# Optimization experiments

Hardware: AMD Instinct MI355X
Metric: run time of the kernel (lower is better)

## Reference

```python
import jax, jax.numpy as jnp
import numpy as np

B, T, HID, H = 2, 2048, 2048, 16
D = HID // H  # 128


def apply_rope(x):
    # Faithful port of the torch helper: treats x dims as (B, T, H, D)
    # regardless of the caller's actual layout (this reproduces the
    # original module's quirk of rotating q along the head axis).
    b, t, h, d = x.shape
    half = d // 2
    x1, x2 = x[..., :half], x[..., half:]
    theta = 1.0 / (10000.0 ** (jnp.arange(0, half, 2, dtype=jnp.float32) / half))
    pos = jnp.arange(t, dtype=jnp.float32)
    freq = pos[:, None] * theta[None, :]            # (t, half//2)
    sin = jnp.sin(freq)[None, :, None, :]
    cos = jnp.cos(freq)[None, :, None, :]
    x1e, x1o = x1[..., ::2], x1[..., 1::2]
    x2e, x2o = x2[..., ::2], x2[..., 1::2]
    x1r = jnp.concatenate([x1e * cos - x1o * sin, x1e * sin + x1o * cos], axis=-1)
    x2r = jnp.concatenate([x2e * cos - x2o * sin, x2e * sin + x2o * cos], axis=-1)
    return jnp.concatenate([x1r, x2r], axis=-1)


def setup_inputs() -> dict:
    key = jax.random.key(0)
    ks = jax.random.split(key, 5)
    s = 0.02
    return {
        "hidden_states": jax.random.normal(ks[0], (B, T, HID), dtype=jnp.float32),
        "Wq": jax.random.normal(ks[1], (HID, HID), dtype=jnp.float32) * s,
        "Wk": jax.random.normal(ks[2], (D, HID), dtype=jnp.float32) * s,
        "Wv": jax.random.normal(ks[3], (D, HID), dtype=jnp.float32) * s,
        "Wo": jax.random.normal(ks[4], (HID, HID), dtype=jnp.float32) * s,
    }


def reference(hidden_states, Wq, Wk, Wv, Wo):
    b, t, _ = hidden_states.shape
    scaling = D ** -0.5
    # projections (nn.Linear: x @ W.T)
    q = (hidden_states @ Wq.T).reshape(b, t, H, D).transpose(0, 2, 1, 3)  # (B,H,T,D)
    k = hidden_states @ Wk.T                                             # (B,T,D)
    v = hidden_states @ Wv.T                                             # (B,T,D)
    # RoPE applied exactly as in the torch module (note layout quirk)
    q = apply_rope(q)                 # rotated along head axis, as original
    k = apply_rope(k[:, None])        # (B,1,T,D): pos=0 -> permutation only
    v = v[:, None]                    # (B,1,T,D)
    scores = jnp.einsum("bhqd,bokd->bhqk", q, k) * scaling  # (B,H,T,T)
    causal = jnp.tril(jnp.ones((t, t), dtype=bool))
    scores = jnp.where(causal[None, None], scores, -jnp.inf)
    probs = jax.nn.softmax(scores, axis=-1)
    attn = jnp.einsum("bhqk,bokd->bhqd", probs, v)           # (B,H,T,D)
    attn = attn.transpose(0, 2, 1, 3).reshape(b, t, HID)
    return attn @ Wo.T
```

## Files before the change

kernel.cpp:

```cpp
#include <hip/hip_runtime.h>
#include <math.h>


typedef unsigned short u16;
typedef __attribute__((ext_vector_type(8))) short s16x8;
typedef __attribute__((ext_vector_type(4))) float f32x4;

#define B_   2
#define T_   2048
#define HID_ 2048
#define H_   16
#define D_   128

__device__ __forceinline__ u16 f2bf(float f) {
  unsigned u = __float_as_uint(f);
  unsigned r = ((u >> 16) & 1u) + 0x7fffu;
  return (u16)((u + r) >> 16);
}
__device__ __forceinline__ float bf2f(u16 b) {
  return __uint_as_float(((unsigned)b) << 16);
}

__global__ void cast_f32_to_bf16(const float* __restrict__ in,
                                 u16* __restrict__ out, int n4) {
  int i = blockIdx.x * blockDim.x + threadIdx.x;
  if (i >= n4) return;
  float4 v = reinterpret_cast<const float4*>(in)[i];
  ushort4 o;
  o.x = f2bf(v.x); o.y = f2bf(v.y); o.z = f2bf(v.z); o.w = f2bf(v.w);
  reinterpret_cast<ushort4*>(out)[i] = o;
}

__device__ __forceinline__ void gload_lds16(const u16* g, u16* lds) {
  __builtin_amdgcn_global_load_lds(
      (const __attribute__((address_space(1))) void*)g,
      (__attribute__((address_space(3))) void*)lds, 16, 0, 0);
}

template <int OUT_BF16>
__global__ __launch_bounds__(256) void gemm_bt(
    const u16* __restrict__ A, const u16* __restrict__ Bm,
    void* __restrict__ Cv, int M, int N, int K) {
  __shared__ __align__(16) u16 As[128 * 64];
  __shared__ __align__(16) u16 Bs[128 * 64];
  const int tid = threadIdx.x;
  const int w = tid >> 6, l = tid & 63;
  const int bm = blockIdx.x, bn = blockIdx.y;
  const int wm = (w >> 1) * 64, wn = (w & 1) * 64;
  const int lg = l >> 4, lc = l & 15;
  const int srow = l >> 3, slot = l & 7;
  f32x4 acc[4][4] = {};

  for (int k0 = 0; k0 < K; k0 += 64) {
#pragma unroll
    for (int i = 0; i < 4; ++i) {
      int R = (w * 4 + i) * 8;
      int row = R + srow;
      int c = slot ^ (row & 7);
      gload_lds16(A + (size_t)(bm * 128 + row) * K + k0 + c * 8, &As[R * 64]);
      gload_lds16(Bm + (size_t)(bn * 128 + row) * K + k0 + c * 8, &Bs[R * 64]);
    }
    __syncthreads();
#pragma unroll
    for (int kc = 0; kc < 2; ++kc) {
      s16x8 af[4], bfv[4];
#pragma unroll
      for (int mi = 0; mi < 4; ++mi) {
        int r = wm + mi * 16 + lc;
        int cc = kc * 4 + lg;
        af[mi] = *(const s16x8*)((const char*)As + r * 128 + ((cc ^ (r & 7)) * 16));
      }
#pragma unroll
      for (int ni = 0; ni < 4; ++ni) {
        int r = wn + ni * 16 + lc;
        int cc = kc * 4 + lg;
        bfv[ni] = *(const s16x8*)((const char*)Bs + r * 128 + ((cc ^ (r & 7)) * 16));
      }
#pragma unroll
      for (int mi = 0; mi < 4; ++mi)
#pragma unroll
        for (int ni = 0; ni < 4; ++ni)
          acc[mi][ni] = __builtin_amdgcn_mfma_f32_16x16x32_bf16(
              af[mi], bfv[ni], acc[mi][ni], 0, 0, 0);
    }
    __syncthreads();
  }
#pragma unroll
  for (int mi = 0; mi < 4; ++mi)
#pragma unroll
    for (int ni = 0; ni < 4; ++ni) {
      int mrow = bm * 128 + wm + mi * 16 + lg * 4;
      int ncol = bn * 128 + wn + ni * 16 + lc;
#pragma unroll
      for (int r = 0; r < 4; ++r) {
        float v = acc[mi][ni][r];
        if (OUT_BF16)
          ((u16*)Cv)[(size_t)(mrow + r) * N + ncol] = f2bf(v);
        else
          ((float*)Cv)[(size_t)(mrow + r) * N + ncol] = v;
      }
    }
}

__global__ void rope_q(u16* __restrict__ Q) {
  int idx = blockIdx.x * blockDim.x + threadIdx.x;
  int row = idx >> 10;
  int p = idx & 1023;
  int h = p >> 6;
  int i = p & 63;
  int j = i & 31;
  int d = (i < 32) ? (2 * i) : (64 + 2 * (i - 32));
  float theta = exp2f(-(float)j * (13.287712379549449f / 32.0f));
  float ang = (float)h * theta;
  float s, c;
  __sincosf(ang, &s, &c);
  unsigned* pq = (unsigned*)(Q + (size_t)row * HID_ + h * D_ + d);
  unsigned v = *pq;
  float a = bf2f((u16)(v & 0xffffu));
  float b = bf2f((u16)(v >> 16));
  *pq = ((unsigned)f2bf(a * s + b * c) << 16) | (unsigned)f2bf(a * c - b * s);
}

__global__ void transpose_v(const u16* __restrict__ V, u16* __restrict__ Vt) {
  int idx = blockIdx.x * blockDim.x + threadIdx.x;
  int t = idx & (T_ - 1);
  int d = (idx >> 11) & (D_ - 1);
  int b = idx >> 18;
  Vt[idx] = V[(size_t)(b * T_ + t) * D_ + d];
}

__global__ __launch_bounds__(256) void mqa_attn(
    const u16* __restrict__ Q, const u16* __restrict__ K,
    const u16* __restrict__ Vt, u16* __restrict__ O) {
  __shared__ __align__(16) u16 Plds[4][16][72];
  const int tid = threadIdx.x;
  const int w = tid >> 6, l = tid & 63;
  const int lg = l >> 4, lc = l & 15;
  const int pj = blockIdx.x >> 1, half = blockIdx.x & 1;
  const int h = blockIdx.y, b = blockIdx.z;
  const int tile = (w < 2) ? pj : (31 - pj);
  const int q0 = tile * 64 + half * 32 + (w & 1) * 16;
  const u16* Kb = K + (size_t)b * T_ * D_;
  const u16* Vb = Vt + (size_t)b * D_ * T_;

  s16x8 qf[4];
  const u16* qbase = Q + (size_t)(b * T_ + q0 + lc) * HID_ + h * D_ + lg * 8;
#pragma unroll
  for (int kc = 0; kc < 4; ++kc) qf[kc] = *(const s16x8*)(qbase + kc * 32);

  float mR[4], ls[4];
  f32x4 acc[8] = {};
#pragma unroll
  for (int r = 0; r < 4; ++r) { mR[r] = -INFINITY; ls[r] = 0.f; }
  const float scale = 0.08838834764831845f;
  const int qmax = q0 + 15;
  const int nk64 = qmax / 64 + 1;

  for (int kt = 0; kt < nk64; ++kt) {
    const int kb = kt * 64;
    f32x4 sac[4];
#pragma unroll
    for (int s = 0; s < 4; ++s) {
      f32x4 a = {0.f, 0.f, 0.f, 0.f};
      const u16* kp = Kb + (size_t)(kb + s * 16 + lc) * D_ + lg * 8;
#pragma unroll
      for (int kc = 0; kc < 4; ++kc) {
        s16x8 kf = *(const s16x8*)(kp + kc * 32);
        a = __builtin_amdgcn_mfma_f32_16x16x32_bf16(qf[kc], kf, a, 0, 0, 0);
      }
      sac[s] = a;
    }
    s16x8 vf0[8];
#pragma unroll
    for (int dt = 0; dt < 8; ++dt)
      vf0[dt] = *(const s16x8*)(Vb + (size_t)(dt * 16 + lc) * T_ + kb + lg * 8);
    const bool lastc = (kt == nk64 - 1);
    float sv[4][4], pm[4];
#pragma unroll
    for (int r = 0; r < 4; ++r) {
      const int qabs = q0 + lg * 4 + r;
#pragma unroll
      for (int s = 0; s < 4; ++s) {
        float x = sac[s][r] * scale;
        if (lastc && (kb + s * 16 + lc > qabs)) x = -INFINITY;
        sv[s][r] = x;
      }
      pm[r] = fmaxf(fmaxf(sv[0][r], sv[1][r]), fmaxf(sv[2][r], sv[3][r]));
    }
#pragma unroll
    for (int m = 1; m < 16; m <<= 1)
#pragma unroll
      for (int r = 0; r < 4; ++r)
        pm[r] = fmaxf(pm[r], __shfl_xor(pm[r], m, 64));
    float fsc[4];
#pragma unroll
    for (int r = 0; r < 4; ++r) {
      float nm = fmaxf(mR[r], pm[r]);
      fsc[r] = __expf(mR[r] - nm);
      float acc_l = 0.f;
#pragma unroll
      for (int s = 0; s < 4; ++s) {
        float pp = __expf(sv[s][r] - nm);
        acc_l += pp;
        Plds[w][lg * 4 + r][s * 16 + lc] = f2bf(pp);
      }
      ls[r] = ls[r] * fsc[r] + acc_l;
      mR[r] = nm;
    }
#pragma unroll
    for (int dt = 0; dt < 8; ++dt) {
      f32x4 a = acc[dt];
#pragma unroll
      for (int r = 0; r < 4; ++r) a[r] *= fsc[r];
      acc[dt] = a;
    }
    s16x8 pa0 = *(const s16x8*)&Plds[w][lc][lg * 8];
#pragma unroll
    for (int dt = 0; dt < 8; ++dt)
      acc[dt] = __builtin_amdgcn_mfma_f32_16x16x32_bf16(pa0, vf0[dt], acc[dt], 0, 0, 0);
    s16x8 pa1 = *(const s16x8*)&Plds[w][lc][32 + lg * 8];
#pragma unroll
    for (int dt = 0; dt < 8; ++dt) {
      s16x8 vf = *(const s16x8*)(Vb + (size_t)(dt * 16 + lc) * T_ + kb + 32 + lg * 8);
      acc[dt] = __builtin_amdgcn_mfma_f32_16x16x32_bf16(pa1, vf, acc[dt], 0, 0, 0);
    }
  }
#pragma unroll
  for (int m = 1; m < 16; m <<= 1)
#pragma unroll
    for (int r = 0; r < 4; ++r)
      ls[r] += __shfl_xor(ls[r], m, 64);
  u16* ob = O + (size_t)(b * T_ + q0 + lg * 4) * HID_ + h * D_ + lc;
#pragma unroll
  for (int dt = 0; dt < 8; ++dt)
#pragma unroll
    for (int r = 0; r < 4; ++r)
      ob[(size_t)r * HID_ + dt * 16] = f2bf(acc[dt][r] / ls[r]);
}

extern "C" void kernel_launch(void* const* d_in, const int* in_sizes, int n_in,
                              void* d_out, int out_size, void* d_ws, size_t ws_size,
                              hipStream_t stream) {
  const float* hs = (const float*)d_in[0];
  const float* Wq = (const float*)d_in[1];
  const float* Wk = (const float*)d_in[2];
  const float* Wv = (const float*)d_in[3];
  const float* Wo = (const float*)d_in[4];
  float* out = (float*)d_out;
  char* ws = (char*)d_ws;

  u16* hb  = (u16*)(ws + 0);
  u16* wqb = (u16*)(ws + 16777216);
  u16* wkb = (u16*)(ws + 25165824);
  u16* wvb = (u16*)(ws + 25690112);
  u16* wob = (u16*)(ws + 26214400);
  u16* Qb  = (u16*)(ws + 34603008);
  u16* Kb  = (u16*)(ws + 51380224);
  u16* Vb  = (u16*)(ws + 52428800);
  u16* Vtb = (u16*)(ws + 53477376);
  u16* Ab  = (u16*)(ws + 54525952);

  cast_f32_to_bf16<<<8192, 256, 0, stream>>>(hs, hb, 2097152);
  cast_f32_to_bf16<<<4096, 256, 0, stream>>>(Wq, wqb, 1048576);
  cast_f32_to_bf16<<<256, 256, 0, stream>>>(Wk, wkb, 65536);
  cast_f32_to_bf16<<<256, 256, 0, stream>>>(Wv, wvb, 65536);
  cast_f32_to_bf16<<<4096, 256, 0, stream>>>(Wo, wob, 1048576);

  gemm_bt<1><<<dim3(32, 16), 256, 0, stream>>>(hb, wqb, Qb, 4096, 2048, 2048);
  gemm_bt<1><<<dim3(32, 1), 256, 0, stream>>>(hb, wkb, Kb, 4096, 128, 2048);
  gemm_bt<1><<<dim3(32, 1), 256, 0, stream>>>(hb, wvb, Vb, 4096, 128, 2048);

  rope_q<<<16384, 256, 0, stream>>>(Qb);
  transpose_v<<<2048, 256, 0, stream>>>(Vb, Vtb);

  mqa_attn<<<dim3(32, 16, 2), 256, 0, stream>>>(Qb, Kb, Vtb, Ab);

  gemm_bt<0><<<dim3(32, 16), 256, 0, stream>>>(Ab, wob, out, 4096, 2048, 2048);

  (void)in_sizes; (void)n_in; (void)out_size; (void)ws_size;
}
```

Baseline: 436.2 us.

## Pair causal-balanced query tiles per wave to share K/V loads in attention

Each wave now handles two 16-row query tiles, one near the start and one near the end of the sequence (idx and 127-idx). The two tiles share each K and V fragment load, with the shorter tile's work skipped once its causal range is done. This halves the grid and balances causal work per wave, while reusing K/V register loads across two MFMA streams. In exchange register pressure roughly doubles (two accumulator sets), and launch bounds now request 2 blocks per CU, which may force spills or lower occupancy.

Result: no change. 431.8 us (-1.0%).

```diff
diff --git a/kernel.cpp b/kernel.cpp
--- a/kernel.cpp
+++ b/kernel.cpp
@@ -129,113 +129,217 @@
   Vt[idx] = V[(size_t)(b * T_ + t) * D_ + d];
 }
 
-__global__ __launch_bounds__(256) void mqa_attn(
+__global__ __launch_bounds__(256, 2) void mqa_attn(
     const u16* __restrict__ Q, const u16* __restrict__ K,
     const u16* __restrict__ Vt, u16* __restrict__ O) {
-  __shared__ __align__(16) u16 Plds[4][16][72];
+  __shared__ __align__(16) u16 Plds[4][2][16][72];
   const int tid = threadIdx.x;
   const int w = tid >> 6, l = tid & 63;
   const int lg = l >> 4, lc = l & 15;
-  const int pj = blockIdx.x >> 1, half = blockIdx.x & 1;
+  const int idx = blockIdx.x * 4 + w;
   const int h = blockIdx.y, b = blockIdx.z;
-  const int tile = (w < 2) ? pj : (31 - pj);
-  const int q0 = tile * 64 + half * 32 + (w & 1) * 16;
-  const u16* Kb = K + (size_t)b * T_ * D_;
+  const int ga = idx, gb = 127 - idx;
+  const int q0a = ga * 16, q0b = gb * 16;
+  const int nka = ga / 4 + 1, nkb = gb / 4 + 1;
+  const u16* Kp = K + (size_t)b * T_ * D_;
   const u16* Vb = Vt + (size_t)b * D_ * T_;
 
-  s16x8 qf[4];
-  const u16* qbase = Q + (size_t)(b * T_ + q0 + lc) * HID_ + h * D_ + lg * 8;
-#pragma unroll
-  for (int kc = 0; kc < 4; ++kc) qf[kc] = *(const s16x8*)(qbase + kc * 32);
-
-  float mR[4], ls[4];
-  f32x4 acc[8] = {};
-#pragma unroll
-  for (int r = 0; r < 4; ++r) { mR[r] = -INFINITY; ls[r] = 0.f; }
+  s16x8 qfa[4], qfb[4];
+  {
+    const u16* qa = Q + (size_t)(b * T_ + q0a + lc) * HID_ + h * D_ + lg * 8;
+    const u16* qb = Q + (size_t)(b * T_ + q0b + lc) * HID_ + h * D_ + lg * 8;
+#pragma unroll
+    for (int kc = 0; kc < 4; ++kc) {
+      qfa[kc] = *(const s16x8*)(qa + kc * 32);
+      qfb[kc] = *(const s16x8*)(qb + kc * 32);
+    }
+  }
+
+  float mA[4], lA[4], mB[4], lB[4];
+  f32x4 accA[8] = {}, accB[8] = {};
+#pragma unroll
+  for (int r = 0; r < 4; ++r) { mA[r] = -INFINITY; lA[r] = 0.f; mB[r] = -INFINITY; lB[r] = 0.f; }
   const float scale = 0.08838834764831845f;
-  const int qmax = q0 + 15;
-  const int nk64 = qmax / 64 + 1;
-
-  for (int kt = 0; kt < nk64; ++kt) {
+
+  for (int kt = 0; kt < nkb; ++kt) {
     const int kb = kt * 64;
-    f32x4 sac[4];
-#pragma unroll
-    for (int s = 0; s < 4; ++s) {
-      f32x4 a = {0.f, 0.f, 0.f, 0.f};
-      const u16* kp = Kb + (size_t)(kb + s * 16 + lc) * D_ + lg * 8;
-#pragma unroll
-      for (int kc = 0; kc < 4; ++kc) {
-        s16x8 kf = *(const s16x8*)(kp + kc * 32);
-        a = __builtin_amdgcn_mfma_f32_16x16x32_bf16(qf[kc], kf, a, 0, 0, 0);
-      }
-      sac[s] = a;
+    const bool doA = (kt < nka);
+    f32x4 sacA[4], sacB[4];
+    if (doA) {
+#pragma unroll
+      for (int s = 0; s < 4; ++s) {
+        const u16* kp = Kp + (size_t)(kb + s * 16 + lc) * D_ + lg * 8;
+        s16x8 kf0 = *(const s16x8*)(kp);
+        s16x8 kf1 = *(const s16x8*)(kp + 32);
+        s16x8 kf2 = *(const s16x8*)(kp + 64);
+        s16x8 kf3 = *(const s16x8*)(kp + 96);
+        f32x4 aB = {0.f, 0.f, 0.f, 0.f};
+        aB = __builtin_amdgcn_mfma_f32_16x16x32_bf16(qfb[0], kf0, aB, 0, 0, 0);
+        aB = __builtin_amdgcn_mfma_f32_16x16x32_bf16(qfb[1], kf1, aB, 0, 0, 0);
+        aB = __builtin_amdgcn_mfma_f32_16x16x32_bf16(qfb[2], kf2, aB, 0, 0, 0);
+        aB = __builtin_amdgcn_mfma_f32_16x16x32_bf16(qfb[3], kf3, aB, 0, 0, 0);
+        sacB[s] = aB;
+        f32x4 aA = {0.f, 0.f, 0.f, 0.f};
+        aA = __builtin_amdgcn_mfma_f32_16x16x32_bf16(qfa[0], kf0, aA, 0, 0, 0);
+        aA = __builtin_amdgcn_mfma_f32_16x16x32_bf16(qfa[1], kf1, aA, 0, 0, 0);
+        aA = __builtin_amdgcn_mfma_f32_16x16x32_bf16(qfa[2], kf2, aA, 0, 0, 0);
+        aA = __builtin_amdgcn_mfma_f32_16x16x32_bf16(qfa[3], kf3, aA, 0, 0, 0);
+        sacA[s] = aA;
+      }
+    } else {
+#pragma unroll
+      for (int s = 0; s < 4; ++s) {
+        const u16* kp = Kp + (size_t)(kb + s * 16 + lc) * D_ + lg * 8;
+        s16x8 kf0 = *(const s16x8*)(kp);
+        s16x8 kf1 = *(const s16x8*)(kp + 32);
+        s16x8 kf2 = *(const s16x8*)(kp + 64);
+        s16x8 kf3 = *(const s16x8*)(kp + 96);
+        f32x4 aB = {0.f, 0.f, 0.f, 0.f};
+        aB = __builtin_amdgcn_mfma_f32_16x16x32_bf16(qfb[0], kf0, aB, 0, 0, 0);
+        aB = __builtin_amdgcn_mfma_f32_16x16x32_bf16(qfb[1], kf1, aB, 0, 0, 0);
+        aB = __builtin_amdgcn_mfma_f32_16x16x32_bf16(qfb[2], kf2, aB, 0, 0, 0);
+        aB = __builtin_amdgcn_mfma_f32_16x16x32_bf16(qfb[3], kf3, aB, 0, 0, 0);
+        sacB[s] = aB;
+      }
     }
     s16x8 vf0[8];
 #pragma unroll
     for (int dt = 0; dt < 8; ++dt)
       vf0[dt] = *(const s16x8*)(Vb + (size_t)(dt * 16 + lc) * T_ + kb + lg * 8);
-    const bool lastc = (kt == nk64 - 1);
-    float sv[4][4], pm[4];
+    {
+      const bool lastc = (kt == nkb - 1);
+      float sv[4][4], pm[4];
+#pragma unroll
+      for (int r = 0; r < 4; ++r) {
+        const int qabs = q0b + lg * 4 + r;
+#pragma unroll
+        for (int s = 0; s < 4; ++s) {
+          float x = sacB[s][r] * scale;
+          if (lastc && (kb + s * 16 + lc > qabs)) x = -INFINITY;
+          sv[s][r] = x;
+        }
+        pm[r] = fmaxf(fmaxf(sv[0][r], sv[1][r]), fmaxf(sv[2][r], sv[3][r]));
+      }
+#pragma unroll
+      for (int m = 1; m < 16; m <<= 1)
+#pragma unroll
+        for (int r = 0; r < 4; ++r)
+          pm[r] = fmaxf(pm[r], __shfl_xor(pm[r], m, 64));
+      float fsc[4];
+#pragma unroll
+      for (int r = 0; r < 4; ++r) {
+        float nm = fmaxf(mB[r], pm[r]);
+        fsc[r] = __expf(mB[r] - nm);
+        float al = 0.f;
+#pragma unroll
+        for (int s = 0; s < 4; ++s) {
+          float pp = __expf(sv[s][r] - nm);
+          al += pp;
+          Plds[w][1][lg * 4 + r][s * 16 + lc] = f2bf(pp);
+        }
+        lB[r] = lB[r] * fsc[r] + al;
+        mB[r] = nm;
+      }
+#pragma unroll
+      for (int dt = 0; dt < 8; ++dt) {
+        f32x4 a = accB[dt];
+#pragma unroll
+        for (int r = 0; r < 4; ++r) a[r] *= fsc[r];
+        accB[dt] = a;
+      }
+    }
+    if (doA) {
+      const bool lastc = (kt == nka - 1);
+      float sv[4][4], pm[4];
+#pragma unroll
+      for (int r = 0; r < 4; ++r) {
+        const int qabs = q0a + lg * 4 + r;
+#pragma unroll
+        for (int s = 0; s < 4; ++s) {
+          float x = sacA[s][r] * scale;
+          if (lastc && (kb + s * 16 + lc > qabs)) x = -INFINITY;
+          sv[s][r] = x;
+        }
+        pm[r] = fmaxf(fmaxf(sv[0][r], sv[1][r]), fmaxf(sv[2][r], sv[3][r]));
+      }
+#pragma unroll
+      for (int m = 1; m < 16; m <<= 1)
+#pragma unroll
+        for (int r = 0; r < 4; ++r)
+          pm[r] = fmaxf(pm[r], __shfl_xor(pm[r], m, 64));
+      float fsc[4];
+#pragma unroll
+      for (int r = 0; r < 4; ++r) {
+        float nm = fmaxf(mA[r], pm[r]);
+        fsc[r] = __expf(mA[r] - nm);
+        float al = 0.f;
+#pragma unroll
+        for (int s = 0; s < 4; ++s) {
+          float pp = __expf(sv[s][r] - nm);
+          al += pp;
+          Plds[w][0][lg * 4 + r][s * 16 + lc] = f2bf(pp);
+        }
+        lA[r] = lA[r] * fsc[r] + al;
+        mA[r] = nm;
+      }
+#pragma unroll
+      for (int dt = 0; dt < 8; ++dt) {
+        f32x4 a = accA[dt];
+#pragma unroll
+        for (int r = 0; r < 4; ++r) a[r] *= fsc[r];
+        accA[dt] = a;
+      }
+    }
+    {
+      s16x8 paB = *(const s16x8*)&Plds[w][1][lc][lg * 8];
+      if (doA) {
+        s16x8 paA = *(const s16x8*)&Plds[w][0][lc][lg * 8];
+#pragma unroll
+        for (int dt = 0; dt < 8; ++dt) {
+          accB[dt] = __builtin_amdgcn_mfma_f32_16x16x32_bf16(paB, vf0[dt], accB[dt], 0, 0, 0);
+          accA[dt] = __builtin_amdgcn_mfma_f32_16x16x32_bf16(paA, vf0[dt], accA[dt], 0, 0, 0);
+        }
+      } else {
+#pragma unroll
+        for (int dt = 0; dt < 8; ++dt)
+          accB[dt] = __builtin_amdgcn_mfma_f32_16x16x32_bf16(paB, vf0[dt], accB[dt], 0, 0, 0);
+      }
+    }
+    {
+      s16x8 paB = *(const s16x8*)&Plds[w][1][lc][32 + lg * 8];
+      if (doA) {
+        s16x8 paA = *(const s16x8*)&Plds[w][0][lc][32 + lg * 8];
+#pragma unroll
+        for (int dt = 0; dt < 8; ++dt) {
+          s16x8 vf = *(const s16x8*)(Vb + (size_t)(dt * 16 + lc) * T_ + kb + 32 + lg * 8);
+          accB[dt] = __builtin_amdgcn_mfma_f32_16x16x32_bf16(paB, vf, accB[dt], 0, 0, 0);
+          accA[dt] = __builtin_amdgcn_mfma_f32_16x16x32_bf16(paA, vf, accA[dt], 0, 0, 0);
+        }
+      } else {
+#pragma unroll
+        for (int dt = 0; dt < 8; ++dt) {
+          s16x8 vf = *(const s16x8*)(Vb + (size_t)(dt * 16 + lc) * T_ + kb + 32 + lg * 8);
+          accB[dt] = __builtin_amdgcn_mfma_f32_16x16x32_bf16(paB, vf, accB[dt], 0, 0, 0);
+        }
+      }
+    }
+  }
+#pragma unroll
+  for (int m = 1; m < 16; m <<= 1)
 #pragma unroll
     for (int r = 0; r < 4; ++r) {
-      const int qabs = q0 + lg * 4 + r;
-#pragma unroll
-      for (int s = 0; s < 4; ++s) {
-        float x = sac[s][r] * scale;
-        if (lastc && (kb + s * 16 + lc > qabs)) x = -INFINITY;
-        sv[s][r] = x;
-      }
-      pm[r] = fmaxf(fmaxf(sv[0][r], sv[1][r]), fmaxf(sv[2][r], sv[3][r]));
-    }
-#pragma unroll
-    for (int m = 1; m < 16; m <<= 1)
-#pragma unroll
-      for (int r = 0; r < 4; ++r)
-        pm[r] = fmaxf(pm[r], __shfl_xor(pm[r], m, 64));
-    float fsc[4];
+      lA[r] += __shfl_xor(lA[r], m, 64);
+      lB[r] += __shfl_xor(lB[r], m, 64);
+    }
+  u16* oa = O + (size_t)(b * T_ + q0a + lg * 4) * HID_ + h * D_ + lc;
+  u16* ob = O + (size_t)(b * T_ + q0b + lg * 4) * HID_ + h * D_ + lc;
+#pragma unroll
+  for (int dt = 0; dt < 8; ++dt)
 #pragma unroll
     for (int r = 0; r < 4; ++r) {
-      float nm = fmaxf(mR[r], pm[r]);
-      fsc[r] = __expf(mR[r] - nm);
-      float acc_l = 0.f;
-#pragma unroll
-      for (int s = 0; s < 4; ++s) {
-        float pp = __expf(sv[s][r] - nm);
-        acc_l += pp;
-        Plds[w][lg * 4 + r][s * 16 + lc] = f2bf(pp);
-      }
-      ls[r] = ls[r] * fsc[r] + acc_l;
-      mR[r] = nm;
-    }
-#pragma unroll
-    for (int dt = 0; dt < 8; ++dt) {
-      f32x4 a = acc[dt];
-#pragma unroll
-      for (int r = 0; r < 4; ++r) a[r] *= fsc[r];
-      acc[dt] = a;
-    }
-    s16x8 pa0 = *(const s16x8*)&Plds[w][lc][lg * 8];
-#pragma unroll
-    for (int dt = 0; dt < 8; ++dt)
-      acc[dt] = __builtin_amdgcn_mfma_f32_16x16x32_bf16(pa0, vf0[dt], acc[dt], 0, 0, 0);
-    s16x8 pa1 = *(const s16x8*)&Plds[w][lc][32 + lg * 8];
-#pragma unroll
-    for (int dt = 0; dt < 8; ++dt) {
-      s16x8 vf = *(const s16x8*)(Vb + (size_t)(dt * 16 + lc) * T_ + kb + 32 + lg * 8);
-      acc[dt] = __builtin_amdgcn_mfma_f32_16x16x32_bf16(pa1, vf, acc[dt], 0, 0, 0);
-    }
-  }
-#pragma unroll
-  for (int m = 1; m < 16; m <<= 1)
-#pragma unroll
-    for (int r = 0; r < 4; ++r)
-      ls[r] += __shfl_xor(ls[r], m, 64);
-  u16* ob = O + (size_t)(b * T_ + q0 + lg * 4) * HID_ + h * D_ + lc;
-#pragma unroll
-  for (int dt = 0; dt < 8; ++dt)
-#pragma unroll
-    for (int r = 0; r < 4; ++r)
-      ob[(size_t)r * HID_ + dt * 16] = f2bf(acc[dt][r] / ls[r]);
+      oa[(size_t)r * HID_ + dt * 16] = f2bf(accA[dt][r] / lA[r]);
+      ob[(size_t)r * HID_ + dt * 16] = f2bf(accB[dt][r] / lB[r]);
+    }
 }
 
 extern "C" void kernel_launch(void* const* d_in, const int* in_sizes, int n_in,
@@ -273,7 +377,7 @@
   rope_q<<<16384, 256, 0, stream>>>(Qb);
   transpose_v<<<2048, 256, 0, stream>>>(Vb, Vtb);
 
-  mqa_attn<<<dim3(32, 16, 2), 256, 0, stream>>>(Qb, Kb, Vtb, Ab);
+  mqa_attn<<<dim3(16, 16, 2), 256, 0, stream>>>(Qb, Kb, Vtb, Ab);
 
   gemm_bt<0><<<dim3(32, 16), 256, 0, stream>>>(Ab, wob, out, 4096, 2048, 2048);
 
```
